# Kernel optimization log

Hardware: AMD Instinct MI355X
Metric: run time of the kernel (lower is better)

The kernel has to match this reference:

```python
import jax, jax.numpy as jnp
import numpy as np

NUM_HEADS = 8
GROUPS = 32
EPS = 1e-5


def setup_inputs() -> dict:
    key = jax.random.key(0)
    k1, k2, k3 = jax.random.split(key, 3)
    B, C, H, W = 16, 512, 64, 64
    x = jax.random.normal(k1, (B, C, H, W), dtype=jnp.float32)
    scale = C ** -0.5  # keep qkv/proj outputs well-scaled
    return {
        "x": x,
        "norm_w": jnp.ones((C,), jnp.float32),
        "norm_b": jnp.zeros((C,), jnp.float32),
        "qkv_w": jax.random.normal(k2, (3 * C, C), dtype=jnp.float32) * scale,
        "qkv_b": jnp.zeros((3 * C,), jnp.float32),
        "proj_w": jax.random.normal(k3, (C, C), dtype=jnp.float32) * scale,
        "proj_b": jnp.zeros((C,), jnp.float32),
    }


def reference(x, norm_w, norm_b, qkv_w, qkv_b, proj_w, proj_b):
    B, C, H, W = x.shape
    N = H * W
    nh = NUM_HEADS
    hd = C // nh

    # GroupNorm(32, C)
    xg = x.reshape(B, GROUPS, C // GROUPS, N)
    mu = xg.mean(axis=(2, 3), keepdims=True)
    var = xg.var(axis=(2, 3), keepdims=True)
    h = ((xg - mu) * jax.lax.rsqrt(var + EPS)).reshape(B, C, N)
    h = h * norm_w[None, :, None] + norm_b[None, :, None]

    h = h.transpose(0, 2, 1)  # [B, N, C]
    qkv = (h @ qkv_w.T + qkv_b).reshape(B, N, 3, nh, hd)
    q, k, v = qkv[:, :, 0], qkv[:, :, 1], qkv[:, :, 2]  # each [B, N, nh, hd]

    # Faithful to source: attention over the HEAD axis at each position
    attn = jnp.einsum('bnhd,bngd->bnhg', q, k) * (hd ** -0.5)  # [B, N, nh, nh]
    attn = jax.nn.softmax(attn, axis=-1)
    o = jnp.einsum('bnhg,bngd->bnhd', attn, v).reshape(B, N, C)

    o = o @ proj_w.T + proj_b  # [B, N, C]
    return x + o.transpose(0, 2, 1).reshape(B, C, H, W)
```

## Files before the change

kernel.cpp:

```cpp
#include <hip/hip_runtime.h>

typedef __attribute__((ext_vector_type(8))) short short8v;
typedef __attribute__((ext_vector_type(4))) float float4v;
typedef unsigned short ushortT;

__device__ __forceinline__ unsigned short f2bf(float f) {
  union { float f; unsigned u; } a; a.f = f;
  unsigned r = a.u + 0x7fffu + ((a.u >> 16) & 1u);
  return (unsigned short)(r >> 16);
}
__device__ __forceinline__ float2 up2(unsigned u) {
  union { unsigned u; float f; } a, b;
  a.u = u << 16; b.u = u & 0xffff0000u;
  return make_float2(a.f, b.f);
}
__device__ __forceinline__ void gl_lds16(const void* g, void* l) {
  __builtin_amdgcn_global_load_lds(
      (const __attribute__((address_space(1))) void*)g,
      (__attribute__((address_space(3))) void*)l, 16, 0, 0);
}

#define WAITV4 asm volatile("s_waitcnt vmcnt(4)" ::: "memory")
#define WAITV0 asm volatile("s_waitcnt vmcnt(0)" ::: "memory")
#define BAR()  __builtin_amdgcn_s_barrier()
#define MFMA16(d, a, b) d = __builtin_amdgcn_mfma_f32_16x16x32_bf16(a, b, d, 0, 0, 0)

__global__ __launch_bounds__(256) void prep(const float* __restrict__ qkvw,
                                            const float* __restrict__ pw,
                                            const float* __restrict__ x,
                                            ushortT* __restrict__ wq_b,
                                            ushortT* __restrict__ wp_b,
                                            float2* __restrict__ stats) {
  int bid = blockIdx.x, tid = threadIdx.x;
  if (bid < 1024) {
    const float* src = (bid < 768) ? qkvw : pw;
    ushortT* dst     = (bid < 768) ? wq_b : wp_b;
    int base = (bid < 768) ? bid : (bid - 768);
    int i = (base * 256 + tid) * 4;
    float4 v = *(const float4*)(src + i);
    uint2 o;
    o.x = (unsigned)f2bf(v.x) | ((unsigned)f2bf(v.y) << 16);
    o.y = (unsigned)f2bf(v.z) | ((unsigned)f2bf(v.w) << 16);
    *(uint2*)(dst + i) = o;
    return;
  }
  int bg = bid - 1024;
  const float* base = x + (size_t)bg * 65536;
  float s = 0.f, s2 = 0.f;
  for (int i = tid; i < 16384; i += 256) {
    float4 v = *(const float4*)(base + (size_t)i * 4);
    s  += v.x + v.y + v.z + v.w;
    s2 += v.x * v.x + v.y * v.y + v.z * v.z + v.w * v.w;
  }
  #pragma unroll
  for (int off = 32; off > 0; off >>= 1) {
    s  += __shfl_down(s, off);
    s2 += __shfl_down(s2, off);
  }
  __shared__ float red[8];
  int w = tid >> 6, l = tid & 63;
  if (l == 0) { red[w] = s; red[w + 4] = s2; }
  __syncthreads();
  if (tid == 0) {
    float ts = red[0] + red[1] + red[2] + red[3];
    float t2 = red[4] + red[5] + red[6] + red[7];
    float mean = ts * (1.f / 65536.f);
    float var  = t2 * (1.f / 65536.f) - mean * mean;
    stats[bg] = make_float2(mean, rsqrtf(var + 1e-5f));
  }
}

__global__ __launch_bounds__(512) void norm_tr(const float* __restrict__ x,
                                               const float* __restrict__ nw,
                                               const float* __restrict__ nb,
                                               const float2* __restrict__ stats,
                                               ushortT* __restrict__ h) {
  __shared__ float t[64][65];
  int n0 = blockIdx.x * 64, c0 = blockIdx.y * 64, b = blockIdx.z;
  int tx = threadIdx.x, ty = threadIdx.y;
  #pragma unroll
  for (int j = ty; j < 64; j += 8) {
    int c = c0 + j;
    float2 ms = stats[b * 32 + (c >> 4)];
    float v = x[((size_t)b * 512 + c) * 4096 + n0 + tx];
    t[j][tx] = (v - ms.x) * ms.y * nw[c] + nb[c];
  }
  __syncthreads();
  #pragma unroll
  for (int j = ty; j < 64; j += 8) {
    int n = n0 + j;
    h[((size_t)b * 4096 + n) * 512 + c0 + tx] = f2bf(t[tx][j]);
  }
}

__device__ __forceinline__ void core256b(const ushortT* __restrict__ A,
                                         const ushortT* __restrict__ Bm,
                                         ushortT* lds, int m0, int n0,
                                         float4v (&acc)[8][4]) {
  char* ldsb = (char*)lds;
  const int tid = threadIdx.x;
  const int w = tid >> 6, l = tid & 63;
  const int wm = w >> 2, wn = w & 3;

  const int P0b = tid * 16, P1b = 8192 + tid * 16;
  const int r0 = P0b >> 7, r1 = P1b >> 7;
  const int s0 = (P0b & 127) ^ ((r0 & 7) << 4);
  const int s1 = (P1b & 127) ^ ((r1 & 7) << 4);
  const size_t g0 = (size_t)r0 * 512 + (s0 >> 1);
  const size_t g1 = (size_t)r1 * 512 + (s1 >> 1);
  auto stage = [&](const ushortT* mat, int rowbase, int kt, int bufb, int region) {
    const ushortT* gsrc = mat + (size_t)rowbase * 512 + kt * 64;
    char* dbase = ldsb + bufb + region;
    gl_lds16(gsrc + g0, dbase + P0b);
    gl_lds16(gsrc + g1, dbase + P1b);
  };

  const int colb = (l >> 4) * 16;
  const int cs0 = colb ^ ((l & 7) << 4);
  const int cs1 = (64 + colb) ^ ((l & 7) << 4);
  const int arow = wm * 16384 + (l & 15) * 128;
  const int brow = 32768 + wn * 8192 + (l & 15) * 128;

  short8v Af[4][2], Bf[4][2];

  #define RDA4(bb, MH)                                                  \
    { _Pragma("unroll")                                                 \
      for (int mm = 0; mm < 4; ++mm) {                                  \
        const char* p = ldsb + (bb) + arow + ((MH)*4 + mm) * 2048;      \
        Af[mm][0] = *(const short8v*)(p + cs0);                         \
        Af[mm][1] = *(const short8v*)(p + cs1);                         \
      } }
  #define RDB2(bb, N0)                                                  \
    { _Pragma("unroll")                                                 \
      for (int nn = 0; nn < 2; ++nn) {                                  \
        const char* p = ldsb + (bb) + brow + ((N0) + nn) * 2048;        \
        Bf[(N0)+nn][0] = *(const short8v*)(p + cs0);                    \
        Bf[(N0)+nn][1] = *(const short8v*)(p + cs1);                    \
      } }
  #define CLUSTER(MH, NP)                                               \
    { __builtin_amdgcn_s_setprio(1);                                    \
      _Pragma("unroll")                                                 \
      for (int mm = 0; mm < 4; ++mm) {                                  \
        _Pragma("unroll")                                               \
        for (int nn = 0; nn < 2; ++nn) {                                \
          MFMA16(acc[(MH)*4+mm][(NP)*2+nn], Af[mm][0], Bf[(NP)*2+nn][0]); \
          MFMA16(acc[(MH)*4+mm][(NP)*2+nn], Af[mm][1], Bf[(NP)*2+nn][1]); \
        } }                                                             \
      __builtin_amdgcn_s_setprio(0); }

  auto tile = [&](int bb, int t1, int t2, bool s1g, bool s2g, int vw) {
    RDB2(bb, 0); RDA4(bb, 0);
    if (s1g) stage(A, m0 + 128, t1, bb ^ 65536, 16384);
    BAR();
    CLUSTER(0, 0);
    BAR();
    RDB2(bb, 2);
    if (s1g) stage(Bm, n0 + 128, t1, bb ^ 65536, 49152);
    BAR();
    CLUSTER(0, 1);
    BAR();
    RDA4(bb, 1);
    if (s2g) stage(Bm, n0, t2, bb, 32768);
    BAR();
    CLUSTER(1, 1);
    BAR();
    if (s2g) stage(A, m0, t2, bb, 0);
    if (vw == 4)      { WAITV4; }
    else if (vw == 0) { WAITV0; }
    BAR();
    CLUSTER(1, 0);
    BAR();
  };

  stage(A,  m0,       0, 0, 0);
  stage(A,  m0 + 128, 0, 0, 16384);
  stage(Bm, n0,       0, 0, 32768);
  stage(Bm, n0 + 128, 0, 0, 49152);
  stage(Bm, n0,       1, 65536, 32768);
  stage(A,  m0,       1, 65536, 0);
  WAITV4;
  BAR();

  #pragma unroll 1
  for (int tp = 0; tp < 3; ++tp) {
    tile(0,     2 * tp + 1, 2 * tp + 2, true, true, 4);
    tile(65536, 2 * tp + 2, 2 * tp + 3, true, true, 4);
  }
  tile(0,     7, 8, true,  false, 0);
  tile(65536, 8, 9, false, false, -1);
  #undef RDA4
  #undef RDB2
  #undef CLUSTER
}

__global__ __launch_bounds__(512, 2) void gemm_qkv(const ushortT* __restrict__ h,
                                                   const ushortT* __restrict__ wq,
                                                   const float* __restrict__ bias,
                                                   ushortT* __restrict__ outq) {
  __shared__ ushortT lds[65536];
  int bid = blockIdx.x;
  int wg = (bid & 7) * 192 + (bid >> 3);
  int m0 = (wg / 6) * 256, n0 = (wg % 6) * 256;
  float4v acc[8][4] = {};
  core256b(h, wq, lds, m0, n0, acc);
  const int tid = threadIdx.x;
  const int w = tid >> 6, l = tid & 63;
  const int wm = w >> 2, wn = w & 3;
  __syncthreads();
  ushortT* es = lds + w * 1280;
  float bb[4];
  #pragma unroll
  for (int fn = 0; fn < 4; ++fn) bb[fn] = bias[n0 + wn * 64 + fn * 16 + (l & 15)];
  int r = l >> 2, g = l & 3;
  #pragma unroll
  for (int fm = 0; fm < 8; ++fm) {
    #pragma unroll
    for (int fn = 0; fn < 4; ++fn)
      #pragma unroll
      for (int j = 0; j < 4; ++j)
        es[((l >> 4) * 4 + j) * 72 + fn * 16 + (l & 15)] = f2bf(acc[fm][fn][j] + bb[fn]);
    uint4 v0 = *(const uint4*)(es + r * 72 + g * 16);
    uint4 v1 = *(const uint4*)(es + r * 72 + g * 16 + 8);
    size_t mrow = (size_t)m0 + wm * 128 + fm * 16 + r;
    uint4* dst = (uint4*)(outq + mrow * 1536 + n0 + wn * 64 + g * 16);
    dst[0] = v0; dst[1] = v1;
  }
}

__global__ __launch_bounds__(256) void attn_k(const ushortT* __restrict__ qkv,
                                              ushortT* __restrict__ o) {
  int gp = blockIdx.x * 256 + threadIdx.x;
  int pos = gp >> 3, hh = gp & 7;
  const ushortT* base = qkv + (size_t)pos * 1536;
  float q[64];
  #pragma unroll
  for (int i = 0; i < 8; ++i) {
    uint4 u = *(const uint4*)(base + hh * 64 + i * 8);
    float2 t0 = up2(u.x), t1 = up2(u.y), t2 = up2(u.z), t3 = up2(u.w);
    q[i*8+0]=t0.x; q[i*8+1]=t0.y; q[i*8+2]=t1.x; q[i*8+3]=t1.y;
    q[i*8+4]=t2.x; q[i*8+5]=t2.y; q[i*8+6]=t3.x; q[i*8+7]=t3.y;
  }
  float lg[8];
  #pragma unroll
  for (int g = 0; g < 8; ++g) {
    float s = 0.f;
    #pragma unroll
    for (int d8 = 0; d8 < 8; ++d8) {
      uint4 kk = *(const uint4*)(base + 512 + g * 64 + d8 * 8);
      float2 k0 = up2(kk.x), k1 = up2(kk.y), k2 = up2(kk.z), k3 = up2(kk.w);
      s += q[d8*8+0]*k0.x + q[d8*8+1]*k0.y + q[d8*8+2]*k1.x + q[d8*8+3]*k1.y
         + q[d8*8+4]*k2.x + q[d8*8+5]*k2.y + q[d8*8+6]*k3.x + q[d8*8+7]*k3.y;
    }
    lg[g] = s * 0.125f;
  }
  float mx = lg[0];
  #pragma unroll
  for (int g = 1; g < 8; ++g) mx = fmaxf(mx, lg[g]);
  float ssum = 0.f;
  #pragma unroll
  for (int g = 0; g < 8; ++g) { lg[g] = __expf(lg[g] - mx); ssum += lg[g]; }
  float inv = 1.f / ssum;
  #pragma unroll
  for (int g = 0; g < 8; ++g) lg[g] *= inv;
  float oa[64];
  #pragma unroll
  for (int i = 0; i < 64; ++i) oa[i] = 0.f;
  #pragma unroll
  for (int g = 0; g < 8; ++g) {
    float wg = lg[g];
    #pragma unroll
    for (int d8 = 0; d8 < 8; ++d8) {
      uint4 vv = *(const uint4*)(base + 1024 + g * 64 + d8 * 8);
      float2 v0 = up2(vv.x), v1 = up2(vv.y), v2 = up2(vv.z), v3 = up2(vv.w);
      oa[d8*8+0] += wg*v0.x; oa[d8*8+1] += wg*v0.y;
      oa[d8*8+2] += wg*v1.x; oa[d8*8+3] += wg*v1.y;
      oa[d8*8+4] += wg*v2.x; oa[d8*8+5] += wg*v2.y;
      oa[d8*8+6] += wg*v3.x; oa[d8*8+7] += wg*v3.y;
    }
  }
  ushortT* dst = o + (size_t)pos * 512 + hh * 64;
  #pragma unroll
  for (int i = 0; i < 8; ++i) {
    uint4 w_;
    w_.x = (unsigned)f2bf(oa[i*8+0]) | ((unsigned)f2bf(oa[i*8+1]) << 16);
    w_.y = (unsigned)f2bf(oa[i*8+2]) | ((unsigned)f2bf(oa[i*8+3]) << 16);
    w_.z = (unsigned)f2bf(oa[i*8+4]) | ((unsigned)f2bf(oa[i*8+5]) << 16);
    w_.w = (unsigned)f2bf(oa[i*8+6]) | ((unsigned)f2bf(oa[i*8+7]) << 16);
    *(uint4*)(dst + i * 8) = w_;
  }
}

__global__ __launch_bounds__(512, 2) void gemm_proj(const ushortT* __restrict__ o,
                                                    const ushortT* __restrict__ wp,
                                                    const float* __restrict__ bias,
                                                    const float* __restrict__ x,
                                                    float* __restrict__ out) {
  __shared__ ushortT lds[65536];
  int bid = blockIdx.x;
  int wg = (bid & 7) * 64 + (bid >> 3);
  int m0 = (wg >> 1) * 256, n0 = (wg & 1) * 256;
  float4v acc[8][4] = {};
  core256b(o, wp, lds, m0, n0, acc);
  const int tid = threadIdx.x;
  const int w = tid >> 6, l = tid & 63;
  const int wm = w >> 2, wn = w & 3;
  __syncthreads();
  float* es = (float*)((char*)lds + w * 4608);
  int b = m0 >> 12;
  int c = n0 + wn * 64 + l;
  float bc = bias[c];
  const float* xrow = x + ((size_t)b * 512 + c) * 4096;
  float* orow = out + ((size_t)b * 512 + c) * 4096;
  int nb0 = (m0 & 4095) + wm * 128;
  #pragma unroll
  for (int fm = 0; fm < 8; ++fm) {
    #pragma unroll
    for (int fn = 0; fn < 4; ++fn)
      #pragma unroll
      for (int j = 0; j < 4; ++j)
        es[((l >> 4) * 4 + j) * 68 + fn * 16 + (l & 15)] = acc[fm][fn][j];
    int nb = nb0 + fm * 16;
    #pragma unroll
    for (int q4 = 0; q4 < 4; ++q4) {
      float4 xv = *(const float4*)(xrow + nb + q4 * 4);
      float4 ov;
      ov.x = xv.x + bc + es[(q4 * 4 + 0) * 68 + l];
      ov.y = xv.y + bc + es[(q4 * 4 + 1) * 68 + l];
      ov.z = xv.z + bc + es[(q4 * 4 + 2) * 68 + l];
      ov.w = xv.w + bc + es[(q4 * 4 + 3) * 68 + l];
      *(float4*)(orow + nb + q4 * 4) = ov;
    }
  }
}

extern "C" void kernel_launch(void* const* d_in, const int* in_sizes, int n_in,
                              void* d_out, int out_size, void* d_ws, size_t ws_size,
                              hipStream_t stream) {
  const float* x     = (const float*)d_in[0];
  const float* nw    = (const float*)d_in[1];
  const float* nb    = (const float*)d_in[2];
  const float* qkvw  = (const float*)d_in[3];
  const float* qkvb  = (const float*)d_in[4];
  const float* pw    = (const float*)d_in[5];
  const float* pb    = (const float*)d_in[6];
  float* out = (float*)d_out;
  char* ws = (char*)d_ws;

  const size_t OFF_WQ   = 4096;
  const size_t OFF_WP   = OFF_WQ + 1572864;
  const size_t OFF_H    = OFF_WP + 524288;
  const size_t OFF_QKV  = OFF_H + 67108864;

  float2* stats   = (float2*)ws;
  ushortT* wq_b   = (ushortT*)(ws + OFF_WQ);
  ushortT* wp_b   = (ushortT*)(ws + OFF_WP);
  ushortT* h      = (ushortT*)(ws + OFF_H);
  ushortT* qkv    = (ushortT*)(ws + OFF_QKV);

  prep<<<1536, 256, 0, stream>>>(qkvw, pw, x, wq_b, wp_b, stats);
  norm_tr<<<dim3(64, 8, 16), dim3(64, 8), 0, stream>>>(x, nw, nb, stats, h);
  gemm_qkv<<<1536, 512, 0, stream>>>(h, wq_b, qkvb, qkv);
  attn_k<<<2048, 256, 0, stream>>>(qkv, h);
  gemm_proj<<<512, 512, 0, stream>>>(h, wp_b, pb, x, out);
}
```

Before: 397.7 us.

## Fuse head-axis attention with output projection GEMM and residual add

Merges the attention kernel and the projection GEMM into one kernel. Each 256-thread block computes attention outputs for 32 positions, stages them as bf16 in LDS, and multiplies them by the projection weights with MFMA, reading weights straight from global memory. It then adds bias and the residual before writing the output. This removes the round trip of the attention output through global memory and one kernel launch. In exchange each block re-reads the whole 512x512 projection weight, relying on cache, and uses small 32-row tiles with lower MFMA efficiency.

Result: slower. 533.9 us (+34.3%).

```diff
diff --git a/kernel.cpp b/kernel.cpp
--- a/kernel.cpp
+++ b/kernel.cpp
@@ -227,11 +227,17 @@
   }
 }
 
-__global__ __launch_bounds__(256) void attn_k(const ushortT* __restrict__ qkv,
-                                              ushortT* __restrict__ o) {
-  int gp = blockIdx.x * 256 + threadIdx.x;
-  int pos = gp >> 3, hh = gp & 7;
-  const ushortT* base = qkv + (size_t)pos * 1536;
+__global__ __launch_bounds__(256) void attn_proj(const ushortT* __restrict__ qkv,
+                                                 const ushortT* __restrict__ wp,
+                                                 const float* __restrict__ pb,
+                                                 const float* __restrict__ x,
+                                                 float* __restrict__ out) {
+  __shared__ ushortT abuf[32 * 516];
+  const int tid = threadIdx.x;
+  const int p0 = blockIdx.x * 32;
+  const int pl = tid >> 3, hh = tid & 7;
+  const ushortT* base = qkv + (size_t)(p0 + pl) * 1536;
+
   float q[64];
   #pragma unroll
   for (int i = 0; i < 8; ++i) {
@@ -278,57 +284,71 @@
       oa[d8*8+6] += wg*v3.x; oa[d8*8+7] += wg*v3.y;
     }
   }
-  ushortT* dst = o + (size_t)pos * 512 + hh * 64;
-  #pragma unroll
-  for (int i = 0; i < 8; ++i) {
-    uint4 w_;
-    w_.x = (unsigned)f2bf(oa[i*8+0]) | ((unsigned)f2bf(oa[i*8+1]) << 16);
-    w_.y = (unsigned)f2bf(oa[i*8+2]) | ((unsigned)f2bf(oa[i*8+3]) << 16);
-    w_.z = (unsigned)f2bf(oa[i*8+4]) | ((unsigned)f2bf(oa[i*8+5]) << 16);
-    w_.w = (unsigned)f2bf(oa[i*8+6]) | ((unsigned)f2bf(oa[i*8+7]) << 16);
-    *(uint4*)(dst + i * 8) = w_;
-  }
-}
-
-__global__ __launch_bounds__(512, 2) void gemm_proj(const ushortT* __restrict__ o,
-                                                    const ushortT* __restrict__ wp,
-                                                    const float* __restrict__ bias,
-                                                    const float* __restrict__ x,
-                                                    float* __restrict__ out) {
-  __shared__ ushortT lds[65536];
-  int bid = blockIdx.x;
-  int wg = (bid & 7) * 64 + (bid >> 3);
-  int m0 = (wg >> 1) * 256, n0 = (wg & 1) * 256;
-  float4v acc[8][4] = {};
-  core256b(o, wp, lds, m0, n0, acc);
-  const int tid = threadIdx.x;
+
+  unsigned* arw = (unsigned*)(abuf + pl * 516 + hh * 64);
+  #pragma unroll
+  for (int ii = 0; ii < 32; ++ii) {
+    int i = (ii + hh * 4) & 31;
+    arw[i] = (unsigned)f2bf(oa[2 * i]) | ((unsigned)f2bf(oa[2 * i + 1]) << 16);
+  }
+  __syncthreads();
+
   const int w = tid >> 6, l = tid & 63;
-  const int wm = w >> 2, wn = w & 3;
-  __syncthreads();
-  float* es = (float*)((char*)lds + w * 4608);
-  int b = m0 >> 12;
-  int c = n0 + wn * 64 + l;
-  float bc = bias[c];
-  const float* xrow = x + ((size_t)b * 512 + c) * 4096;
-  float* orow = out + ((size_t)b * 512 + c) * 4096;
-  int nb0 = (m0 & 4095) + wm * 128;
-  #pragma unroll
-  for (int fm = 0; fm < 8; ++fm) {
-    #pragma unroll
-    for (int fn = 0; fn < 4; ++fn)
+  const int cb0 = w * 128;
+  const char* abb = (const char*)abuf;
+  const int ar0 = (l & 15) * 1032 + (l >> 4) * 16;
+  const int ar1 = (16 + (l & 15)) * 1032 + (l >> 4) * 16;
+  const ushortT* wbase = wp + (size_t)(cb0 + (l & 15)) * 512 + (l >> 4) * 8;
+
+  float4v acc[2][8] = {};
+  short8v BX[8], BY[8];
+  #pragma unroll
+  for (int nf = 0; nf < 8; ++nf)
+    BX[nf] = *(const short8v*)(wbase + (size_t)nf * 16 * 512);
+  #pragma unroll 1
+  for (int kk = 0; kk < 16; kk += 2) {
+    #pragma unroll
+    for (int nf = 0; nf < 8; ++nf)
+      BY[nf] = *(const short8v*)(wbase + (size_t)nf * 16 * 512 + (kk + 1) * 32);
+    short8v A0 = *(const short8v*)(abb + ar0 + kk * 64);
+    short8v A1 = *(const short8v*)(abb + ar1 + kk * 64);
+    #pragma unroll
+    for (int nf = 0; nf < 8; ++nf) {
+      MFMA16(acc[0][nf], A0, BX[nf]);
+      MFMA16(acc[1][nf], A1, BX[nf]);
+    }
+    if (kk + 2 < 16) {
       #pragma unroll
-      for (int j = 0; j < 4; ++j)
-        es[((l >> 4) * 4 + j) * 68 + fn * 16 + (l & 15)] = acc[fm][fn][j];
-    int nb = nb0 + fm * 16;
-    #pragma unroll
-    for (int q4 = 0; q4 < 4; ++q4) {
-      float4 xv = *(const float4*)(xrow + nb + q4 * 4);
+      for (int nf = 0; nf < 8; ++nf)
+        BX[nf] = *(const short8v*)(wbase + (size_t)nf * 16 * 512 + (kk + 2) * 32);
+    }
+    A0 = *(const short8v*)(abb + ar0 + kk * 64 + 64);
+    A1 = *(const short8v*)(abb + ar1 + kk * 64 + 64);
+    #pragma unroll
+    for (int nf = 0; nf < 8; ++nf) {
+      MFMA16(acc[0][nf], A0, BY[nf]);
+      MFMA16(acc[1][nf], A1, BY[nf]);
+    }
+  }
+
+  const int b = p0 >> 12;
+  const int nloc = p0 & 4095;
+  #pragma unroll
+  for (int nf = 0; nf < 8; ++nf) {
+    const int c = cb0 + nf * 16 + (l & 15);
+    const float bc = pb[c];
+    const size_t roff = ((size_t)b * 512 + c) * 4096 + nloc + (l >> 4) * 4;
+    const float* xr = x + roff;
+    float* orow = out + roff;
+    #pragma unroll
+    for (int mf = 0; mf < 2; ++mf) {
+      float4 xv = *(const float4*)(xr + mf * 16);
       float4 ov;
-      ov.x = xv.x + bc + es[(q4 * 4 + 0) * 68 + l];
-      ov.y = xv.y + bc + es[(q4 * 4 + 1) * 68 + l];
-      ov.z = xv.z + bc + es[(q4 * 4 + 2) * 68 + l];
-      ov.w = xv.w + bc + es[(q4 * 4 + 3) * 68 + l];
-      *(float4*)(orow + nb + q4 * 4) = ov;
+      ov.x = xv.x + bc + acc[mf][nf][0];
+      ov.y = xv.y + bc + acc[mf][nf][1];
+      ov.z = xv.z + bc + acc[mf][nf][2];
+      ov.w = xv.w + bc + acc[mf][nf][3];
+      *(float4*)(orow + mf * 16) = ov;
     }
   }
 }
@@ -360,6 +380,5 @@
   prep<<<1536, 256, 0, stream>>>(qkvw, pw, x, wq_b, wp_b, stats);
   norm_tr<<<dim3(64, 8, 16), dim3(64, 8), 0, stream>>>(x, nw, nb, stats, h);
   gemm_qkv<<<1536, 512, 0, stream>>>(h, wq_b, qkvb, qkv);
-  attn_k<<<2048, 256, 0, stream>>>(qkv, h);
-  gemm_proj<<<512, 512, 0, stream>>>(h, wp_b, pb, x, out);
-}
+  attn_proj<<<2048, 256, 0, stream>>>(qkv, wp_b, pb, x, out);
+}
```
